# Kernel tuning notes

Hardware: AMD Instinct MI355X
Metric: run time of the kernel (lower is better)

Reference implementation:

```python
import jax, jax.numpy as jnp
import numpy as np

WS = 7            # window size
NUM_HEADS = 16
DIM = 512
B_ = 4096         # num_windows * batch
NW = 1024         # windows per image
N = WS * WS


def _relative_position_index(ws=WS):
    # static int index table, computed exactly as in the torch module
    coords = np.stack(np.meshgrid(np.arange(ws), np.arange(ws), indexing='ij'))  # (2, ws, ws)
    coords = coords.reshape(2, -1)                                               # (2, N)
    rel = coords[:, :, None] - coords[:, None, :]                                # (2, N, N)
    rel = rel.transpose(1, 2, 0).astype(np.int64)                                # (N, N, 2)
    rel[:, :, 0] += ws - 1
    rel[:, :, 1] += ws - 1
    rel[:, :, 0] *= 2 * ws - 1
    return jnp.asarray(rel.sum(-1))                                              # (N, N)


def setup_inputs() -> dict:
    key = jax.random.key(0)
    ks = jax.random.split(key, 12)
    C = DIM
    std = 0.02
    inp = {
        'local_features': jax.random.normal(ks[0], (B_, N, C), jnp.float32),
        'global_features': jax.random.normal(ks[1], (B_, N, C), jnp.float32),
        'mask': jnp.zeros((NW, N, N), jnp.float32),  # 0/-inf shifted-window mask (all-visible here)
        'bias_table': std * jax.random.normal(ks[2], ((2 * WS - 1) * (2 * WS - 1), NUM_HEADS), jnp.float32),
        'Wk': std * jax.random.normal(ks[3], (C, C), jnp.float32),
        'bk': jnp.zeros((C,), jnp.float32),
        'Wq': std * jax.random.normal(ks[4], (C, C), jnp.float32),
        'bq': jnp.zeros((C,), jnp.float32),
        'Wv': std * jax.random.normal(ks[5], (C, C), jnp.float32),
        'bv': jnp.zeros((C,), jnp.float32),
        'Wp': std * jax.random.normal(ks[6], (C, C), jnp.float32),
        'bp': jnp.zeros((C,), jnp.float32),
    }
    return inp


def reference(local_features, global_features, mask, bias_table,
              Wk, bk, Wq, bq, Wv, bv, Wp, bp):
    Bw, n, C = local_features.shape
    h = NUM_HEADS
    d = C // h
    scale = d ** -0.5

    def heads(x, W, b):
        # torch Linear: x @ W.T + b ; then (B_, N, h, d) -> (B_, h, N, d)
        y = jnp.einsum('bnc,oc->bno', x, W) + b
        return y.reshape(Bw, n, h, d).transpose(0, 2, 1, 3)

    k = heads(local_features, Wk, bk)
    q = heads(global_features, Wq, bq) * scale
    v = heads(local_features, Wv, bv)

    attn = jnp.einsum('bhnd,bhmd->bhnm', q, k)                    # (B_, h, N, N)

    idx = _relative_position_index()                               # (N, N) static
    rpb = bias_table[idx]                                          # (N, N, h)
    attn = attn + rpb.transpose(2, 0, 1)[None]                     # add (1, h, N, N)

    nW = mask.shape[0]
    attn = attn.reshape(Bw // nW, nW, h, n, n) + mask[None, :, None]
    attn = attn.reshape(Bw, h, n, n)
    attn = jax.nn.softmax(attn, axis=-1)

    x = jnp.einsum('bhnm,bhmd->bnhd', attn, v).reshape(Bw, n, C)
    x = jnp.einsum('bnc,oc->bno', x, Wp) + bp
    return x
```

## Files before the change

kernel.cpp:

```cpp
#include <hip/hip_runtime.h>
#include <hip/hip_bf16.h>

typedef __hip_bfloat16 bf16;
typedef __attribute__((ext_vector_type(4))) float f32x4;
typedef __attribute__((ext_vector_type(8))) short short8;
typedef __attribute__((ext_vector_type(4))) short short4v;

#define NEGBIG (-3.0e38f)

__device__ __forceinline__ unsigned short f2b(float x) {
  union { float f; unsigned int u; } v; v.f = x;
  unsigned int r = v.u + 0x7fffu + ((v.u >> 16) & 1u);
  return (unsigned short)(r >> 16);
}

__device__ __forceinline__ void gl16(const void* g, void* l) {
  __builtin_amdgcn_global_load_lds(
      (const __attribute__((address_space(1))) unsigned int*)g,
      (__attribute__((address_space(3))) unsigned int*)l, 16, 0, 0);
}

__device__ __forceinline__ int xcd_swz(int orig, int nwg) {
  const int q = nwg >> 3, r = nwg & 7;
  const int xcd = orig & 7;
  const int base = (xcd < r) ? xcd * (q + 1) : r * (q + 1) + (xcd - r) * q;
  return base + (orig >> 3);
}

__device__ __forceinline__ void stage256(const char* Ab, const char* Bb,
                                         char* buf, int arow0, int brow0,
                                         int k0) {
  const int tid = threadIdx.x;
#pragma unroll
  for (int i = 0; i < 2; ++i) {
    const int g = tid + 512 * i;
    const int row = g >> 2;
    const int scol = ((g & 3) ^ ((row >> 1) & 3)) << 4;
    gl16(Ab + (size_t)(arow0 + row) * 1024 + k0 * 2 + scol, buf + g * 16);
    gl16(Bb + (size_t)(brow0 + row) * 1024 + k0 * 2 + scol,
         buf + 16384 + g * 16);
  }
}

__global__ __launch_bounds__(256) void cvt_w_kernel(
    const float* __restrict__ a, const float* __restrict__ b,
    const float* __restrict__ c, const float* __restrict__ d,
    bf16* __restrict__ dst) {
  const int t = blockIdx.x * 256 + threadIdx.x;
  const float* srcs[4] = {a, b, c, d};
#pragma unroll
  for (int w = 0; w < 4; ++w) {
    const f32x4 v = *(const f32x4*)(srcs[w] + (size_t)t * 4);
    short4v o;
    o[0] = (short)f2b(v[0]); o[1] = (short)f2b(v[1]);
    o[2] = (short)f2b(v[2]); o[3] = (short)f2b(v[3]);
    *(short4v*)((short*)dst + (size_t)w * 262144 + (size_t)t * 4) = o;
  }
}

__global__ __launch_bounds__(256) void cvt_a(const float* __restrict__ src,
                                             short* __restrict__ dst, int M) {
  const int g = blockIdx.x * 256 + threadIdx.x;
  const int row = g >> 6, k8 = g & 63;
  if (row >= M) return;
  const float* sp = src + (size_t)row * 512 + k8 * 8;
  const f32x4 lo = *(const f32x4*)sp;
  const f32x4 hi = *(const f32x4*)(sp + 4);
  short8 u;
  u[0] = (short)f2b(lo[0]); u[1] = (short)f2b(lo[1]);
  u[2] = (short)f2b(lo[2]); u[3] = (short)f2b(lo[3]);
  u[4] = (short)f2b(hi[0]); u[5] = (short)f2b(hi[1]);
  u[6] = (short)f2b(hi[2]); u[7] = (short)f2b(hi[3]);
  *(short8*)(dst + (size_t)row * 512 + k8 * 8) = u;
}

__global__ __launch_bounds__(256) void prep_rpbL(const float* __restrict__ btab,
                                                 float* __restrict__ rpbL) {
  const int g = blockIdx.x * 256 + threadIdx.x;
  const int lane = g & 63, mn = (g >> 6) & 15, h = g >> 10;
  const int m = mn >> 2, n = mn & 3, l15 = lane & 15, lg = lane >> 4;
  const int cc = n * 16 + l15;
  const int aj = cc / 7, bj = cc % 7;
  f32x4 o;
#pragma unroll
  for (int reg = 0; reg < 4; ++reg) {
    const int i = m * 16 + lg * 4 + reg;
    if (i < 49 && cc < 49) {
      const int t = (i / 7 - aj + 6) * 13 + (i % 7 - bj + 6);
      o[reg] = btab[t * 16 + h];
    } else {
      o[reg] = NEGBIG;
    }
  }
  ((f32x4*)rpbL)[g] = o;
}

__global__ __launch_bounds__(256) void prep_maskL(const float* __restrict__ mask,
                                                  float* __restrict__ maskL) {
  const int g = blockIdx.x * 256 + threadIdx.x;
  const int lane = g & 63, mn = (g >> 6) & 15, wm = g >> 10;
  const int m = mn >> 2, n = mn & 3, l15 = lane & 15, lg = lane >> 4;
  const int cc = n * 16 + l15;
  f32x4 o;
#pragma unroll
  for (int reg = 0; reg < 4; ++reg) {
    const int i = m * 16 + lg * 4 + reg;
    o[reg] = (i < 49 && cc < 49) ? mask[(size_t)wm * 2401 + i * 49 + cc] : 0.f;
  }
  ((f32x4*)maskL)[g] = o;
}

template <int MODE>
__global__ __launch_bounds__(512, 2) void gemm256(
    const short* __restrict__ Al, const short* __restrict__ Ag,
    const short* __restrict__ wbf, const float* __restrict__ bk,
    const float* __restrict__ bq, const float* __restrict__ bv, float qscale,
    bf16* __restrict__ k_ws, bf16* __restrict__ q_ws, bf16* __restrict__ vT_ws,
    float* __restrict__ fout, int M) {
  __shared__ char lds[131072];
  const int nwg = gridDim.x;
  const int t0 = xcd_swz(blockIdx.x, nwg);
  const int NB = (MODE == 0) ? 6 : 2;
  const int bn = t0 % NB, bm = t0 / NB;
  const int cls = (MODE == 0) ? (bn >> 1) : 3;
  const int bnl = bn & 1;
  const int tid = threadIdx.x, lane = tid & 63, wid = tid >> 6;
  const int wr = wid >> 2, wc = wid & 3, l15 = lane & 15, lg = lane >> 4;

  const char* Ab = (const char*)((MODE == 1) ? Al : ((cls == 1) ? Ag : Al));
  const char* Bb = (const char*)(wbf + (size_t)((MODE == 1) ? 3 : cls) * 262144);
  const int am0 = bm * 256, bn0 = bnl * 256;
  const bool swap = (MODE == 0) && (cls == 2);

  f32x4 acc[8][4];
#pragma unroll
  for (int m = 0; m < 8; ++m)
#pragma unroll
    for (int n = 0; n < 4; ++n) acc[m][n] = (f32x4){0.f, 0.f, 0.f, 0.f};

  stage256(Ab, Bb, lds, am0, bn0, 0);
  stage256(Ab, Bb, lds + 32768, am0, bn0, 32);
  asm volatile("s_waitcnt vmcnt(4)" ::: "memory");
  __builtin_amdgcn_s_barrier();
  __builtin_amdgcn_sched_barrier(0);

#pragma unroll 1
  for (int t = 0; t < 16; ++t) {
    if (t + 2 < 16)
      stage256(Ab, Bb, lds + ((t + 2) & 3) * 32768, am0, bn0, (t + 2) * 32);
    const char* base = lds + (t & 3) * 32768;
    const char* fa = swap ? base + 16384 : base;
    const char* fb = swap ? base : base + 16384;
    short8 af[8], bfr[4];
#pragma unroll
    for (int m = 0; m < 8; ++m) {
      const int r = wr * 128 + m * 16 + l15;
      af[m] = *(const short8*)(fa + r * 64 + ((lg ^ ((r >> 1) & 3)) << 4));
    }
#pragma unroll
    for (int n = 0; n < 4; ++n) {
      const int r = wc * 64 + n * 16 + l15;
      bfr[n] = *(const short8*)(fb + r * 64 + ((lg ^ ((r >> 1) & 3)) << 4));
    }
    __builtin_amdgcn_s_setprio(1);
#pragma unroll
    for (int m = 0; m < 8; ++m)
#pragma unroll
      for (int n = 0; n < 4; ++n)
        acc[m][n] = __builtin_amdgcn_mfma_f32_16x16x32_bf16(
            af[m], bfr[n], acc[m][n], 0, 0, 0);
    __builtin_amdgcn_s_setprio(0);
    if (t < 14) {
      asm volatile("s_waitcnt vmcnt(4)" ::: "memory");
    } else if (t == 14) {
      asm volatile("s_waitcnt vmcnt(0)" ::: "memory");
    }
    if (t < 15) {
      __builtin_amdgcn_s_barrier();
      __builtin_amdgcn_sched_barrier(0);
    }
  }

  if (MODE == 1) {
#pragma unroll
    for (int m = 0; m < 8; ++m) {
#pragma unroll
      for (int n = 0; n < 4; ++n) {
        const int c = bn0 + wc * 64 + n * 16 + l15;
        const float bvv = bk[c];
#pragma unroll
        for (int reg = 0; reg < 4; ++reg) {
          const int r = am0 + wr * 128 + m * 16 + lg * 4 + reg;
          if (r < M) fout[(size_t)r * 512 + c] = acc[m][n][reg] + bvv;
        }
      }
    }
  } else if (cls == 2) {
#pragma unroll
    for (int m = 0; m < 8; ++m) {
#pragma unroll
      for (int n = 0; n < 4; ++n) {
        const int tok = am0 + wc * 64 + n * 16 + l15;
        if (tok < M) {
          const int w = tok / 49, nt = tok - w * 49;
#pragma unroll
          for (int reg = 0; reg < 4; ++reg) {
            const int ch = bn0 + wr * 128 + m * 16 + lg * 4 + reg;
            const float v = acc[m][n][reg] + bv[ch];
            const int hh = ch >> 5, dd = ch & 31;
            vT_ws[(((size_t)w * 16 + hh) * 32 + dd) * 64 + nt] =
                __float2bfloat16(v);
          }
        }
      }
    }
  } else {
    const float* bb = (cls == 0) ? bk : bq;
    bf16* dp = (cls == 0) ? k_ws : q_ws;
    const float sc = (cls == 0) ? 1.0f : qscale;
#pragma unroll
    for (int m = 0; m < 8; ++m) {
#pragma unroll
      for (int n = 0; n < 4; ++n) {
        const int c = bn0 + wc * 64 + n * 16 + l15;
        const float bvv = bb[c];
        const int hh = c >> 5, dd = c & 31;
#pragma unroll
        for (int reg = 0; reg < 4; ++reg) {
          const int r = am0 + wr * 128 + m * 16 + lg * 4 + reg;
          if (r < M) {
            const int w = r / 49, nt = r - w * 49;
            dp[(((size_t)w * 16 + hh) * 49 + nt) * 32 + dd] =
                __float2bfloat16((acc[m][n][reg] + bvv) * sc);
          }
        }
      }
    }
  }
}

__global__ __launch_bounds__(256) void attn_win2(
    const bf16* __restrict__ q_ws, const bf16* __restrict__ k_ws,
    const bf16* __restrict__ vT_ws, const float* __restrict__ rpbL,
    const float* __restrict__ maskL, bf16* __restrict__ x_ws, int wstart) {
  __shared__ short sP[4][4096];
  const int tid = threadIdx.x, lane = tid & 63, wid = tid >> 6;
  const int l15 = lane & 15, lg = lane >> 4;
  const int wl = blockIdx.x;
  const int h = blockIdx.y * 4 + wid;
  const int wg = wstart + wl;
  char* Pl = (char*)sP[wid];
  const size_t base = ((size_t)wl * 16 + h) * 1568;
  const short8 z8 = (short8){0, 0, 0, 0, 0, 0, 0, 0};

  short8 qf[4], kf[4];
#pragma unroll
  for (int m = 0; m < 4; ++m) {
    const int r = m * 16 + l15;
    qf[m] = (r < 49) ? *(const short8*)(q_ws + base + r * 32 + lg * 8) : z8;
    kf[m] = (r < 49) ? *(const short8*)(k_ws + base + r * 32 + lg * 8) : z8;
  }
  f32x4 lc[4][4];
#pragma unroll
  for (int m = 0; m < 4; ++m)
#pragma unroll
    for (int n = 0; n < 4; ++n)
      lc[m][n] = __builtin_amdgcn_mfma_f32_16x16x32_bf16(
          qf[m], kf[n], (f32x4){0.f, 0.f, 0.f, 0.f}, 0, 0, 0);

  const f32x4* rbp = (const f32x4*)rpbL + (size_t)h * 1024 + lane;
  const f32x4* mkp = (const f32x4*)maskL + (size_t)(wg & 1023) * 1024 + lane;
#pragma unroll
  for (int m = 0; m < 4; ++m)
#pragma unroll
    for (int n = 0; n < 4; ++n) {
      const int mn = m * 4 + n;
      lc[m][n] += rbp[mn * 64] + mkp[mn * 64];
    }

#pragma unroll
  for (int m = 0; m < 4; ++m) {
#pragma unroll
    for (int reg = 0; reg < 4; ++reg) {
      float vmax = fmaxf(fmaxf(lc[m][0][reg], lc[m][1][reg]),
                         fmaxf(lc[m][2][reg], lc[m][3][reg]));
#pragma unroll
      for (int off = 1; off < 16; off <<= 1)
        vmax = fmaxf(vmax, __shfl_xor(vmax, off, 64));
      float e[4], ssum = 0.f;
#pragma unroll
      for (int n = 0; n < 4; ++n) {
        e[n] = __expf(lc[m][n][reg] - vmax);
        ssum += e[n];
      }
#pragma unroll
      for (int off = 1; off < 16; off <<= 1) ssum += __shfl_xor(ssum, off, 64);
      const float inv = __builtin_amdgcn_rcpf(ssum);
      const int i = m * 16 + lg * 4 + reg;
#pragma unroll
      for (int n = 0; n < 4; ++n) {
        const int cc = n * 16 + l15;
        *(unsigned short*)(Pl + i * 128 + ((2 * cc) ^ ((i & 7) << 4))) =
            f2b(e[n] * inv);
      }
    }
  }

  f32x4 xacc[4][2];
#pragma unroll
  for (int m = 0; m < 4; ++m)
#pragma unroll
    for (int n = 0; n < 2; ++n) xacc[m][n] = (f32x4){0.f, 0.f, 0.f, 0.f};
  const size_t vbase = ((size_t)wl * 16 + h) * 2048;
#pragma unroll
  for (int s = 0; s < 2; ++s) {
    short8 pf[4], vf[2];
#pragma unroll
    for (int m = 0; m < 4; ++m) {
      const int i = m * 16 + l15;
      pf[m] = *(const short8*)(Pl + i * 128 +
                               ((s * 64 + lg * 16) ^ ((i & 7) << 4)));
    }
#pragma unroll
    for (int n = 0; n < 2; ++n) {
      const int dd = n * 16 + l15;
      short8 vv = *(const short8*)(vT_ws + vbase + dd * 64 + s * 32 + lg * 8);
      if (s == 1) {
        if (lg == 3) vv = z8;
        else if (lg == 2) {
          vv[1] = 0; vv[2] = 0; vv[3] = 0; vv[4] = 0;
          vv[5] = 0; vv[6] = 0; vv[7] = 0;
        }
      }
      vf[n] = vv;
    }
#pragma unroll
    for (int m = 0; m < 4; ++m)
#pragma unroll
      for (int n = 0; n < 2; ++n)
        xacc[m][n] = __builtin_amdgcn_mfma_f32_16x16x32_bf16(
            pf[m], vf[n], xacc[m][n], 0, 0, 0);
  }

#pragma unroll
  for (int m = 0; m < 4; ++m)
#pragma unroll
    for (int n = 0; n < 2; ++n)
#pragma unroll
      for (int reg = 0; reg < 4; ++reg) {
        const int i = m * 16 + lg * 4 + reg;
        const int dd = n * 16 + l15;
        *(unsigned short*)(Pl + i * 80 + ((2 * dd) ^ ((i & 3) << 4))) =
            f2b(xacc[m][n][reg]);
      }
#pragma unroll
  for (int g = 0; g < 4; ++g) {
    const int row = g * 16 + (lane >> 2);
    if (row < 49) {
      const short8 xv = *(const short8*)(
          Pl + row * 80 + (((lane & 3) * 16) ^ ((row & 3) << 4)));
      *(short8*)(x_ws + ((size_t)wl * 49 + row) * 512 + h * 32 +
                 (lane & 3) * 8) = xv;
    }
  }
}

extern "C" void kernel_launch(void* const* d_in, const int* in_sizes, int n_in,
                              void* d_out, int out_size, void* d_ws,
                              size_t ws_size, hipStream_t stream) {
  const float* lf   = (const float*)d_in[0];
  const float* gfx  = (const float*)d_in[1];
  const float* mask = (const float*)d_in[2];
  const float* btab = (const float*)d_in[3];
  const float* Wk = (const float*)d_in[4];  const float* bk = (const float*)d_in[5];
  const float* Wq = (const float*)d_in[6];  const float* bq = (const float*)d_in[7];
  const float* Wv = (const float*)d_in[8];  const float* bv = (const float*)d_in[9];
  const float* Wp = (const float*)d_in[10]; const float* bp = (const float*)d_in[11];
  float* out = (float*)d_out;

  char* ws = (char*)d_ws;
  short* wbf = (short*)ws;
  size_t off = (size_t)4 * 262144 * 2;
  float* rpbL = (float*)(ws + off); off += (size_t)16 * 4096 * 4;
  float* maskL = (float*)(ws + off); off += (size_t)1024 * 4096 * 4;

  const size_t perw = 2 * 49 * 1024 + 2 * 50176 + 65536;
  size_t avail = (ws_size > off + 65536) ? ws_size - off - 65536 : 0;
  int CH = (int)((avail > 300000) ? (avail - 262144) / perw : 1);
  if (CH > 4096) CH = 4096;
  if (CH < 1) CH = 1;
  const int RWS = ((CH * 49 + 127) / 128) * 128;

  short* Al = (short*)(ws + off); off += (size_t)RWS * 1024;
  short* Ag = (short*)(ws + off); off += (size_t)RWS * 1024;
  bf16* q_ws = (bf16*)(ws + off); off += (size_t)CH * 50176;
  bf16* k_ws = (bf16*)(ws + off); off += (size_t)CH * 50176;
  bf16* vT_ws = (bf16*)(ws + off); off += (size_t)CH * 65536;
  bf16* x_ws = (bf16*)Al;

  cvt_w_kernel<<<256, 256, 0, stream>>>(Wk, Wq, Wv, Wp, (bf16*)wbf);
  prep_rpbL<<<64, 256, 0, stream>>>(btab, rpbL);
  prep_maskL<<<4096, 256, 0, stream>>>(mask, maskL);

  const float qscale = 0.17677669529663687f;
  for (int wstart = 0; wstart < 4096; wstart += CH) {
    const int nwin = (4096 - wstart < CH) ? (4096 - wstart) : CH;
    const int M = nwin * 49;
    const int gy = (M + 255) / 256;
    const int cg = (M * 64 + 255) / 256;
    cvt_a<<<cg, 256, 0, stream>>>(lf + (size_t)wstart * 25088, Al, M);
    cvt_a<<<cg, 256, 0, stream>>>(gfx + (size_t)wstart * 25088, Ag, M);
    gemm256<0><<<6 * gy, 512, 0, stream>>>(Al, Ag, wbf, bk, bq, bv, qscale,
                                           k_ws, q_ws, vT_ws, nullptr, M);
    attn_win2<<<dim3(nwin, 4), 256, 0, stream>>>(q_ws, k_ws, vT_ws, rpbL,
                                                 maskL, x_ws, wstart);
    gemm256<1><<<2 * gy, 512, 0, stream>>>((const short*)x_ws, nullptr, wbf,
                                           bp, nullptr, nullptr, 1.0f, nullptr,
                                           nullptr, nullptr,
                                           out + (size_t)wstart * 25088, M);
  }
}
```

Baseline: 1.412 ms.

## Restructure GEMM mainloop into double-buffered 64-wide K tiles with ping-pong phases

The GEMM K loop now uses two 64 KB LDS buffers holding 64-wide K slices instead of four 32-wide slices. Each iteration is split into quadrant MFMA phases, with global-to-LDS staging of the next tile interleaved between barriers, in the style of an 8-wave ping-pong schedule. The LDS swizzle changes to an 8-way XOR for the wider rows. The goal is better overlap of loads with MFMA and fewer waitcnt stalls, at the cost of many more barriers per tile; the workspace chunk sizing and row padding are adjusted to 256-row alignment to match.

```diff
diff --git a/kernel.cpp b/kernel.cpp
--- a/kernel.cpp
+++ b/kernel.cpp
@@ -25,21 +25,6 @@
   const int xcd = orig & 7;
   const int base = (xcd < r) ? xcd * (q + 1) : r * (q + 1) + (xcd - r) * q;
   return base + (orig >> 3);
-}
-
-__device__ __forceinline__ void stage256(const char* Ab, const char* Bb,
-                                         char* buf, int arow0, int brow0,
-                                         int k0) {
-  const int tid = threadIdx.x;
-#pragma unroll
-  for (int i = 0; i < 2; ++i) {
-    const int g = tid + 512 * i;
-    const int row = g >> 2;
-    const int scol = ((g & 3) ^ ((row >> 1) & 3)) << 4;
-    gl16(Ab + (size_t)(arow0 + row) * 1024 + k0 * 2 + scol, buf + g * 16);
-    gl16(Bb + (size_t)(brow0 + row) * 1024 + k0 * 2 + scol,
-         buf + 16384 + g * 16);
-  }
 }
 
 __global__ __launch_bounds__(256) void cvt_w_kernel(
@@ -111,13 +96,15 @@
 }
 
 template <int MODE>
-__global__ __launch_bounds__(512, 2) void gemm256(
+__global__ __launch_bounds__(512, 2) void gemm8p(
     const short* __restrict__ Al, const short* __restrict__ Ag,
     const short* __restrict__ wbf, const float* __restrict__ bk,
     const float* __restrict__ bq, const float* __restrict__ bv, float qscale,
     bf16* __restrict__ k_ws, bf16* __restrict__ q_ws, bf16* __restrict__ vT_ws,
     float* __restrict__ fout, int M) {
   __shared__ char lds[131072];
+  char* buf0 = lds;
+  char* buf1 = lds + 65536;
   const int nwg = gridDim.x;
   const int t0 = xcd_swz(blockIdx.x, nwg);
   const int NB = (MODE == 0) ? 6 : 2;
@@ -125,12 +112,24 @@
   const int cls = (MODE == 0) ? (bn >> 1) : 3;
   const int bnl = bn & 1;
   const int tid = threadIdx.x, lane = tid & 63, wid = tid >> 6;
-  const int wr = wid >> 2, wc = wid & 3, l15 = lane & 15, lg = lane >> 4;
-
+  const int l15 = lane & 15, lg = lane >> 4;
+  const int wr = wid >> 2, wc = wid & 3;
   const char* Ab = (const char*)((MODE == 1) ? Al : ((cls == 1) ? Ag : Al));
   const char* Bb = (const char*)(wbf + (size_t)((MODE == 1) ? 3 : cls) * 262144);
   const int am0 = bm * 256, bn0 = bnl * 256;
   const bool swap = (MODE == 0) && (cls == 2);
+  const int famoff = swap ? 32768 : 0;
+  const int fbmoff = swap ? 0 : 32768;
+
+  const int srow = tid >> 3;
+  const int ssl = ((tid & 7) ^ (srow & 7)) << 4;
+
+#define STG_A(dstbuf, u, tk)                                                 \
+  gl16(Ab + (size_t)(am0 + (u) * 64 + srow) * 1024 + (tk) * 128 + ssl,       \
+       (dstbuf) + (u) * 8192 + tid * 16)
+#define STG_B(dstbuf, u, tk)                                                 \
+  gl16(Bb + (size_t)(bn0 + (u) * 64 + srow) * 1024 + (tk) * 128 + ssl,       \
+       (dstbuf) + 32768 + (u) * 8192 + tid * 16)
 
   f32x4 acc[8][4];
 #pragma unroll
@@ -138,48 +137,87 @@
 #pragma unroll
     for (int n = 0; n < 4; ++n) acc[m][n] = (f32x4){0.f, 0.f, 0.f, 0.f};
 
-  stage256(Ab, Bb, lds, am0, bn0, 0);
-  stage256(Ab, Bb, lds + 32768, am0, bn0, 32);
-  asm volatile("s_waitcnt vmcnt(4)" ::: "memory");
-  __builtin_amdgcn_s_barrier();
-  __builtin_amdgcn_sched_barrier(0);
+  short8 af[4][2];
+  short8 bfr[2][2][2];
+
+#define LDA_(cb, mh)                                                         \
+  do {                                                                       \
+    for (int mi = 0; mi < 4; ++mi)                                           \
+      for (int s = 0; s < 2; ++s) {                                          \
+        const int r = wr * 128 + ((mh) * 4 + mi) * 16 + l15;                 \
+        af[mi][s] = *(const short8*)((cb) + famoff + r * 128 +               \
+                                     (((s * 4 + lg) ^ (r & 7)) << 4));       \
+      }                                                                      \
+  } while (0)
+#define LDB_(cb, set, nh)                                                    \
+  do {                                                                       \
+    for (int nj = 0; nj < 2; ++nj)                                           \
+      for (int s = 0; s < 2; ++s) {                                          \
+        const int r = wc * 64 + ((nh) * 2 + nj) * 16 + l15;                  \
+        bfr[set][nj][s] = *(const short8*)((cb) + fbmoff + r * 128 +         \
+                                           (((s * 4 + lg) ^ (r & 7)) << 4)); \
+      }                                                                      \
+  } while (0)
+#define MFMAQ_(mh, nh, set)                                                  \
+  do {                                                                       \
+    __builtin_amdgcn_s_setprio(1);                                           \
+    for (int mi = 0; mi < 4; ++mi)                                           \
+      for (int nj = 0; nj < 2; ++nj)                                         \
+        for (int s = 0; s < 2; ++s)                                          \
+          acc[(mh) * 4 + mi][(nh) * 2 + nj] =                                \
+              __builtin_amdgcn_mfma_f32_16x16x32_bf16(                       \
+                  af[mi][s], bfr[set][nj][s],                                \
+                  acc[(mh) * 4 + mi][(nh) * 2 + nj], 0, 0, 0);               \
+    __builtin_amdgcn_s_setprio(0);                                           \
+  } while (0)
+#define BAR __builtin_amdgcn_s_barrier()
+#define LGK0 asm volatile("s_waitcnt lgkmcnt(0)")
+
+  STG_A(buf0, 0, 0); STG_A(buf0, 1, 0); STG_A(buf0, 2, 0); STG_A(buf0, 3, 0);
+  STG_B(buf0, 0, 0); STG_B(buf0, 1, 0); STG_B(buf0, 2, 0); STG_B(buf0, 3, 0);
+  STG_A(buf1, 0, 1); STG_A(buf1, 1, 1);
+  asm volatile("s_waitcnt vmcnt(2)" ::: "memory");
+  BAR;
 
 #pragma unroll 1
-  for (int t = 0; t < 16; ++t) {
-    if (t + 2 < 16)
-      stage256(Ab, Bb, lds + ((t + 2) & 3) * 32768, am0, bn0, (t + 2) * 32);
-    const char* base = lds + (t & 3) * 32768;
-    const char* fa = swap ? base + 16384 : base;
-    const char* fb = swap ? base : base + 16384;
-    short8 af[8], bfr[4];
-#pragma unroll
-    for (int m = 0; m < 8; ++m) {
-      const int r = wr * 128 + m * 16 + l15;
-      af[m] = *(const short8*)(fa + r * 64 + ((lg ^ ((r >> 1) & 3)) << 4));
-    }
-#pragma unroll
-    for (int n = 0; n < 4; ++n) {
-      const int r = wc * 64 + n * 16 + l15;
-      bfr[n] = *(const short8*)(fb + r * 64 + ((lg ^ ((r >> 1) & 3)) << 4));
-    }
-    __builtin_amdgcn_s_setprio(1);
-#pragma unroll
-    for (int m = 0; m < 8; ++m)
-#pragma unroll
-      for (int n = 0; n < 4; ++n)
-        acc[m][n] = __builtin_amdgcn_mfma_f32_16x16x32_bf16(
-            af[m], bfr[n], acc[m][n], 0, 0, 0);
-    __builtin_amdgcn_s_setprio(0);
-    if (t < 14) {
-      asm volatile("s_waitcnt vmcnt(4)" ::: "memory");
-    } else if (t == 14) {
-      asm volatile("s_waitcnt vmcnt(0)" ::: "memory");
-    }
-    if (t < 15) {
-      __builtin_amdgcn_s_barrier();
-      __builtin_amdgcn_sched_barrier(0);
-    }
-  }
+  for (int it = 0; it < 4; ++it) {
+    const int t1 = 2 * it + 1, t2 = 2 * it + 2, t3 = 2 * it + 3;
+    const bool st = (it < 3);
+    LDA_(buf0, 0); LDB_(buf0, 0, 0);
+    STG_A(buf1, 2, t1); STG_A(buf1, 3, t1);
+    BAR; LGK0; MFMAQ_(0, 0, 0); BAR;
+    LDB_(buf0, 1, 1);
+    STG_B(buf1, 0, t1); STG_B(buf1, 1, t1);
+    BAR; LGK0; MFMAQ_(0, 1, 1); BAR;
+    LDA_(buf0, 1);
+    STG_B(buf1, 2, t1); STG_B(buf1, 3, t1);
+    BAR; LGK0; MFMAQ_(1, 0, 0); BAR;
+    if (st) { STG_A(buf0, 0, t2); STG_A(buf0, 1, t2); }
+    BAR; MFMAQ_(1, 1, 1);
+    if (st) asm volatile("s_waitcnt vmcnt(2)" ::: "memory");
+    else    asm volatile("s_waitcnt vmcnt(0)" ::: "memory");
+    BAR;
+    LDA_(buf1, 0); LDB_(buf1, 0, 0);
+    if (st) { STG_A(buf0, 2, t2); STG_A(buf0, 3, t2); }
+    BAR; LGK0; MFMAQ_(0, 0, 0); BAR;
+    LDB_(buf1, 1, 1);
+    if (st) { STG_B(buf0, 0, t2); STG_B(buf0, 1, t2); }
+    BAR; LGK0; MFMAQ_(0, 1, 1); BAR;
+    LDA_(buf1, 1);
+    if (st) { STG_B(buf0, 2, t2); STG_B(buf0, 3, t2); }
+    BAR; LGK0; MFMAQ_(1, 0, 0); BAR;
+    if (st) { STG_A(buf1, 0, t3); STG_A(buf1, 1, t3); }
+    BAR; MFMAQ_(1, 1, 1);
+    if (st) asm volatile("s_waitcnt vmcnt(2)" ::: "memory");
+    BAR;
+  }
+#undef STG_A
+#undef STG_B
+#undef LDA_
+#undef LDB_
+#undef MFMAQ_
+#undef BAR
+#undef LGK0
 
   if (MODE == 1) {
 #pragma unroll
@@ -386,10 +424,10 @@
 
   const size_t perw = 2 * 49 * 1024 + 2 * 50176 + 65536;
   size_t avail = (ws_size > off + 65536) ? ws_size - off - 65536 : 0;
-  int CH = (int)((avail > 300000) ? (avail - 262144) / perw : 1);
+  int CH = (int)((avail > 600000) ? (avail - 524288) / perw : 1);
   if (CH > 4096) CH = 4096;
   if (CH < 1) CH = 1;
-  const int RWS = ((CH * 49 + 127) / 128) * 128;
+  const int RWS = ((CH * 49 + 255) / 256) * 256;
 
   short* Al = (short*)(ws + off); off += (size_t)RWS * 1024;
   short* Ag = (short*)(ws + off); off += (size_t)RWS * 1024;
@@ -410,13 +448,13 @@
     const int cg = (M * 64 + 255) / 256;
     cvt_a<<<cg, 256, 0, stream>>>(lf + (size_t)wstart * 25088, Al, M);
     cvt_a<<<cg, 256, 0, stream>>>(gfx + (size_t)wstart * 25088, Ag, M);
-    gemm256<0><<<6 * gy, 512, 0, stream>>>(Al, Ag, wbf, bk, bq, bv, qscale,
-                                           k_ws, q_ws, vT_ws, nullptr, M);
+    gemm8p<0><<<6 * gy, 512, 0, stream>>>(Al, Ag, wbf, bk, bq, bv, qscale,
+                                          k_ws, q_ws, vT_ws, nullptr, M);
     attn_win2<<<dim3(nwin, 4), 256, 0, stream>>>(q_ws, k_ws, vT_ws, rpbL,
                                                  maskL, x_ws, wstart);
-    gemm256<1><<<2 * gy, 512, 0, stream>>>((const short*)x_ws, nullptr, wbf,
-                                           bp, nullptr, nullptr, 1.0f, nullptr,
-                                           nullptr, nullptr,
-                                           out + (size_t)wstart * 25088, M);
-  }
-}
+    gemm8p<1><<<2 * gy, 512, 0, stream>>>((const short*)x_ws, nullptr, wbf,
+                                          bp, nullptr, nullptr, 1.0f, nullptr,
+                                          nullptr, nullptr,
+                                          out + (size_t)wstart * 25088, M);
+  }
+}
```

Result: faster. 1.321 ms (-6.5%).
